# Kernel optimization log

Measured on AMD Instinct MI355X. Metric: run time of the kernel, lower is better.

Reference implementation:

```python
import jax, jax.numpy as jnp
import numpy as np

N, E, D, H, G, L, EF = 50000, 800000, 128, 256, 512, 3, 8
BN_EPS = 1e-5


def _bn(h, g, b):
    # torch BatchNorm1d in training mode: biased batch stats over the node axis
    m = h.mean(0)
    v = h.var(0)
    return g * (h - m) * jax.lax.rsqrt(v + BN_EPS) + b


def setup_inputs() -> dict:
    ks = jax.random.split(jax.random.key(0), 12)
    sc = 0.05
    return {
        "x": jax.random.normal(ks[0], (N, D), jnp.float32),
        "edge_attr": jax.random.normal(ks[1], (E, EF), jnp.float32),
        "vn_emb": jnp.zeros((1, D), jnp.float32),  # init.constant_(0)
        "We": jax.random.normal(ks[2], (L, EF, D)) * sc,
        "be": jnp.zeros((L, D)),
        "W1": jax.random.normal(ks[3], (L, D, H)) * sc,
        "b1": jnp.zeros((L, H)),
        "g1": jnp.ones((L, H)),
        "bt1": jnp.zeros((L, H)),
        "W2": jax.random.normal(ks[4], (L, H, D)) * sc,
        "b2": jnp.zeros((L, D)),
        "gb": jnp.ones((L, D)),
        "bb": jnp.zeros((L, D)),
        "Wv1": jax.random.normal(ks[5], (L - 1, D, H)) * sc,
        "bv1": jnp.zeros((L - 1, H)),
        "gv1": jnp.ones((L - 1, H)),
        "btv1": jnp.zeros((L - 1, H)),
        "Wv2": jax.random.normal(ks[6], (L - 1, H, D)) * sc,
        "bv2": jnp.zeros((L - 1, D)),
        "gv2": jnp.ones((L - 1, D)),
        "btv2": jnp.zeros((L - 1, D)),
        "edge_index": jax.random.randint(ks[7], (2, E), 0, N),
        "batch": jnp.sort(jax.random.randint(ks[8], (N,), 0, G)),
    }


def reference(x, edge_attr, vn_emb, We, be, W1, b1, g1, bt1, W2, b2, gb, bb,
              Wv1, bv1, gv1, btv1, Wv2, bv2, gv2, btv2, edge_index, batch):
    src, dst = edge_index[0], edge_index[1]
    vn = jnp.broadcast_to(vn_emb, (G, D))  # Embedding(1, D) looked up for every graph
    h = x  # node_encoder is None -> encoded_node = x
    for l in range(L):
        h_in = h + vn[batch]                              # virtual-node broadcast (gather)
        e = edge_attr @ We[l] + be[l]                     # per-layer edge encoder
        msg = jax.nn.relu(h_in[src] + e)                  # GIN message, [E, D]
        aggr = jax.ops.segment_sum(msg, dst, num_segments=N)
        z = h_in + aggr                                   # (1+eps)*h + aggr, eps=0
        z = jax.nn.relu(_bn(z @ W1[l] + b1[l], g1[l], bt1[l]))
        h = _bn(z @ W2[l] + b2[l], gb[l], bb[l])          # conv MLP out + outer BatchNorm
        if l < L - 1:
            h = jax.nn.relu(h)                            # dropout ratio 0 -> identity
            pooled = jax.ops.segment_sum(h_in, batch, num_segments=G) + vn
            t = jax.nn.relu(_bn(pooled @ Wv1[l] + bv1[l], gv1[l], btv1[l]))
            vn = jax.nn.relu(_bn(t @ Wv2[l] + bv2[l], gv2[l], btv2[l]))
    return h  # JK == 'last'
```

## Files before the change

### kernel.cpp

```cpp
#include <hip/hip_runtime.h>
#include <hip/hip_bf16.h>

#define N_NODES 50000
#define N_EDGES 800000
#define DIM 128
#define HID 256
#define N_GRAPH 512
#define N_LAYER 3
#define EFEAT 8
#define BN_EPS 1e-5f
#define MAX_GROUPS 240000

typedef unsigned short u16;
typedef unsigned int u32;

using bf16x8_t = short __attribute__((ext_vector_type(8)));
using f32x4_t  = float __attribute__((ext_vector_type(4)));
using f32x2    = float __attribute__((ext_vector_type(2)));
using f32x4v   = float __attribute__((ext_vector_type(4)));


__device__ __forceinline__ void atomic_add_f(float* p, float v) {
    unsafeAtomicAdd(p, v);
}
__device__ __forceinline__ u16 f2bf(float x) {
    union { float f; u32 u; } v; v.f = x;
    u32 r = v.u + 0x7FFF + ((v.u >> 16) & 1);
    return (u16)(r >> 16);
}
__device__ __forceinline__ float bf2f(u16 u) {
    union { u32 i; float f; } v; v.i = (u32)u << 16; return v.f;
}
__device__ __forceinline__ float2 up2(u32 p) {
    return make_float2(bf2f((u16)(p & 0xFFFF)), bf2f((u16)(p >> 16)));
}
__device__ __forceinline__ u32 pk2(float a, float b) {
    return (u32)f2bf(a) | ((u32)f2bf(b) << 16);
}
__device__ __forceinline__ float bflo(u32 u) {
    union { u32 i; float f; } v; v.i = u << 16; return v.f;
}
__device__ __forceinline__ float bfhi(u32 u) {
    union { u32 i; float f; } v; v.i = u & 0xFFFF0000u; return v.f;
}
__device__ __forceinline__ f32x2 up2p(u32 p) {
    union { u32 u[2]; f32x2 f; } v;
    v.u[0] = p << 16;
    v.u[1] = p & 0xFFFF0000u;
    return v.f;
}
__device__ __forceinline__ f32x2 splat2(float x) {
    f32x2 r; r.x = x; r.y = x; return r;
}

__global__ __launch_bounds__(256) void wconv_kernel(
    const float* __restrict__ W1, const float* __restrict__ W2,
    u16* __restrict__ W1t, u16* __restrict__ W2t)
{
    int idx = blockIdx.x * 256 + threadIdx.x;
    if (idx >= 6 * 32768) return;
    int m = idx >> 15;
    int off = idx & 32767;
    int l = m >> 1;
    if ((m & 1) == 0) {
        int r = off >> 8, c = off & 255;
        W1t[(size_t)l * 32768 + c * 128 + r] = f2bf(W1[(size_t)l * 32768 + r * 256 + c]);
    } else {
        int r = off >> 7, c = off & 127;
        W2t[(size_t)l * 32768 + c * 256 + r] = f2bf(W2[(size_t)l * 32768 + r * 128 + c]);
    }
}

__global__ __launch_bounds__(256) void hist_rank_kernel(
    const int* __restrict__ ei, int* __restrict__ deg, int* __restrict__ rank)
{
    int e = blockIdx.x * 256 + threadIdx.x;
    if (e >= N_EDGES) return;
    int dst = ei[N_EDGES + e];
    rank[e] = atomicAdd(&deg[dst], 1);
}

__global__ __launch_bounds__(1024) void scan_kernel(const int* __restrict__ deg, int* __restrict__ grpptr) {
    __shared__ int wsum[16];
    __shared__ int carry;
    int tid = threadIdx.x;
    if (tid == 0) { carry = 0; grpptr[0] = 0; }
    __syncthreads();
    for (int base = 0; base < N_NODES; base += 1024) {
        int i = base + tid;
        int v = (i < N_NODES) ? ((deg[i] + 3) >> 2) : 0;
        int lane = tid & 63, w = tid >> 6;
        int s = v;
        #pragma unroll
        for (int d = 1; d < 64; d <<= 1) { int t = __shfl_up(s, d); if (lane >= d) s += t; }
        if (lane == 63) wsum[w] = s;
        __syncthreads();
        if (tid < 64) {
            int t = (tid < 16) ? wsum[tid] : 0;
            #pragma unroll
            for (int d = 1; d < 16; d <<= 1) { int u = __shfl_up(t, d); if (tid >= d) t += u; }
            if (tid < 16) wsum[tid] = t;
        }
        __syncthreads();
        int excl = (w > 0) ? wsum[w - 1] : 0;
        int incl = s + excl + carry;
        if (i < N_NODES) grpptr[i + 1] = incl;
        __syncthreads();
        if (tid == 0) carry += wsum[15];
        __syncthreads();
    }
}

__global__ __launch_bounds__(256) void scatter_kernel(
    const int* __restrict__ ei, const float* __restrict__ ea,
    const int* __restrict__ rank, const int* __restrict__ grpptr,
    char* __restrict__ rec)
{
    int e = blockIdx.x * 256 + threadIdx.x;
    if (e >= N_EDGES) return;
    int src = __builtin_nontemporal_load(ei + e);
    int dst = __builtin_nontemporal_load(ei + N_EDGES + e);
    int rk  = __builtin_nontemporal_load(rank + e);
    int grp = grpptr[dst] + (rk >> 2);
    int j = rk & 3;
    f32x4v lo = __builtin_nontemporal_load((const f32x4v*)(ea + (size_t)e * EFEAT));
    f32x4v hi = __builtin_nontemporal_load((const f32x4v*)(ea + (size_t)e * EFEAT + 4));
    uint4 q;
    q.x = pk2(lo.x, lo.y); q.y = pk2(lo.z, lo.w);
    q.z = pk2(hi.x, hi.y); q.w = pk2(hi.z, hi.w);
    char* rb = rec + (size_t)grp * 80;
    *(uint4*)(rb + 16 + j * 16) = q;
    *(u32*)(rb + j * 4) = (u32)src << 8;
}

template <bool USEBN, int VNM>
__global__ __launch_bounds__(256) void hin_kernel(
    const float* __restrict__ src,
    const float* __restrict__ sum2, const float* __restrict__ ss2,
    const float* __restrict__ g, const float* __restrict__ b, float invN,
    const int* __restrict__ batch,
    const float* __restrict__ vn_emb,
    const float* __restrict__ vnpre, const float* __restrict__ vsum, const float* __restrict__ vss,
    const float* __restrict__ gv, const float* __restrict__ btv, float invG,
    u16* __restrict__ hin, int total4)
{
    int idx = blockIdx.x * 256 + threadIdx.x;
    if (idx >= total4) return;
    int base = idx * 4;
    int n = base >> 7;
    int c = base & (DIM - 1);
    float4 v = *(const float4*)(src + base);
    float o[4] = {v.x, v.y, v.z, v.w};
    if (USEBN) {
        #pragma unroll
        for (int j = 0; j < 4; ++j) {
            int cj = c + j;
            float m = sum2[cj] * invN;
            float var = ss2[cj] * invN - m * m;
            float r = rsqrtf(var + BN_EPS);
            float a = g[cj] * r;
            o[j] = fmaxf(fmaf(a, o[j], b[cj] - m * a), 0.f);
        }
    }
    int grp = batch[n];
    if (VNM == 0) {
        const float4 w = *(const float4*)(vn_emb + c);
        o[0] += w.x; o[1] += w.y; o[2] += w.z; o[3] += w.w;
    } else {
        const float4 vp = *(const float4*)(vnpre + (size_t)grp * DIM + c);
        float vv[4] = {vp.x, vp.y, vp.z, vp.w};
        #pragma unroll
        for (int j = 0; j < 4; ++j) {
            int cj = c + j;
            float m = vsum[cj] * invG;
            float var = vss[cj] * invG - m * m;
            float r = rsqrtf(var + BN_EPS);
            float a = gv[cj] * r;
            o[j] += fmaxf(fmaf(a, vv[j], btv[cj] - m * a), 0.f);
        }
    }
    uint2 pk;
    pk.x = pk2(o[0], o[1]);
    pk.y = pk2(o[2], o[3]);
    *(uint2*)(hin + base) = pk;
}

__device__ __forceinline__ void edge_term2(
    u32 h, uint4 eq, const f32x2* rW, f32x2 rB, f32x2& acc)
{
    f32x2 ex = rB;
    ex = __builtin_elementwise_fma(splat2(bflo(eq.x)), rW[0], ex);
    ex = __builtin_elementwise_fma(splat2(bfhi(eq.x)), rW[1], ex);
    ex = __builtin_elementwise_fma(splat2(bflo(eq.y)), rW[2], ex);
    ex = __builtin_elementwise_fma(splat2(bfhi(eq.y)), rW[3], ex);
    ex = __builtin_elementwise_fma(splat2(bflo(eq.z)), rW[4], ex);
    ex = __builtin_elementwise_fma(splat2(bfhi(eq.z)), rW[5], ex);
    ex = __builtin_elementwise_fma(splat2(bflo(eq.w)), rW[6], ex);
    ex = __builtin_elementwise_fma(splat2(bfhi(eq.w)), rW[7], ex);
    f32x2 s = up2p(h) + ex;
    s = __builtin_elementwise_max(s, splat2(0.f));
    acc += s;
}

__global__ __launch_bounds__(256) void aggr_kernel(
    const int* __restrict__ grpptr, const int* __restrict__ deg,
    const char* __restrict__ rec,
    const float* __restrict__ Wel, const float* __restrict__ bel,
    const u16* __restrict__ hin, u16* __restrict__ z, int nWaves)
{
    const int lane = threadIdx.x & 63;
    const int cb = lane * 4;
    const int wid0 = (blockIdx.x << 2) + (threadIdx.x >> 6);

    f32x2 rW[EFEAT];
    #pragma unroll
    for (int k = 0; k < EFEAT; ++k) {
        float2 t = *(const float2*)(Wel + k * DIM + lane * 2);
        rW[k].x = t.x; rW[k].y = t.y;
    }
    float2 tb = *(const float2*)(bel + lane * 2);
    f32x2 rB; rB.x = tb.x; rB.y = tb.y;

    const char* hinB = (const char*)hin;

    for (int node = __builtin_amdgcn_readfirstlane(wid0); node < N_NODES; node += nWaves) {
        int g0 = grpptr[node];
        int ng = grpptr[node + 1] - g0;
        int dg = deg[node];
        f32x2 acc = up2p(*(const u32*)(hinB + ((u32)node << 8) + cb));

        if (ng > 0) {
            const char* base = rec + (size_t)g0 * 80;
            uint4 so = *(const uint4*)base;
            uint4 e0 = *(const uint4*)(base + 16);
            uint4 e1 = *(const uint4*)(base + 32);
            uint4 e2 = *(const uint4*)(base + 48);
            uint4 e3 = *(const uint4*)(base + 64);
            u32 h0 = *(const u32*)(hinB + so.x + cb);
            u32 h1 = *(const u32*)(hinB + so.y + cb);
            u32 h2 = *(const u32*)(hinB + so.z + cb);
            u32 h3 = *(const u32*)(hinB + so.w + cb);
            uint4 soA = *(const uint4*)(base + 80);
            const char* pn = base + 80;

            #pragma unroll 1
            for (int c = 0; c < ng - 1; ++c) {
                u32 i0 = *(const u32*)(hinB + soA.x + cb);
                u32 i1 = *(const u32*)(hinB + soA.y + cb);
                u32 i2 = *(const u32*)(hinB + soA.z + cb);
                u32 i3 = *(const u32*)(hinB + soA.w + cb);
                uint4 soN = *(const uint4*)(pn + 80);
                uint4 f0 = *(const uint4*)(pn + 16);
                uint4 f1 = *(const uint4*)(pn + 32);
                uint4 f2 = *(const uint4*)(pn + 48);
                uint4 f3 = *(const uint4*)(pn + 64);
                edge_term2(h0, e0, rW, rB, acc);
                edge_term2(h1, e1, rW, rB, acc);
                edge_term2(h2, e2, rW, rB, acc);
                edge_term2(h3, e3, rW, rB, acc);
                h0 = i0; h1 = i1; h2 = i2; h3 = i3;
                e0 = f0; e1 = f1; e2 = f2; e3 = f3;
                soA = soN;
                pn += 80;
            }
            int valid = dg - (ng - 1) * 4;
            edge_term2(h0, e0, rW, rB, acc);
            if (valid > 1) edge_term2(h1, e1, rW, rB, acc);
            if (valid > 2) edge_term2(h2, e2, rW, rB, acc);
            if (valid > 3) edge_term2(h3, e3, rW, rB, acc);
        }
        *(u32*)(z + ((size_t)node << 7) + lane * 2) = pk2(acc.x, acc.y);
    }
}

template <int MODE, bool CBF16>
__global__ __launch_bounds__(256) void gemm_bf16_kernel(
    const u16* __restrict__ Aa,
    const float* __restrict__ sSum, const float* __restrict__ sSS,
    const float* __restrict__ gA, const float* __restrict__ btA, float invCnt,
    const u16* __restrict__ Bt,
    const float* __restrict__ bias,
    void* __restrict__ CoutV,
    float* __restrict__ outSum, float* __restrict__ outSS,
    int M, int K, int Nc)
{
    constexpr int BM = 128, BN = 128, BK = 128;
    constexpr int LDA = BK + 8;
    __shared__ u16 As[BM * LDA];
    __shared__ u16 Bs[64 * LDA];
    __shared__ float csum[BN], css[BN];

    const int tid = threadIdx.x;
    const int wave = tid >> 6, lane = tid & 63;
    const int row0 = blockIdx.x * BM, col0 = blockIdx.y * BN;
    const int w_m = (wave & 1) * 64, w_n = (wave >> 1) * 32;
    const int quad = lane >> 4, l16 = lane & 15;

    if (tid < BN) { csum[tid] = 0.f; css[tid] = 0.f; }

    f32x4_t acc[4][4];
    #pragma unroll
    for (int mi = 0; mi < 4; ++mi)
        #pragma unroll
        for (int ni = 0; ni < 4; ++ni)
            acc[mi][ni] = (f32x4_t){0.f, 0.f, 0.f, 0.f};

    const int kc = (tid & 15) * 8;
    const int nkt = K / BK;

    for (int kt = 0; kt < nkt; ++kt) {
        float af[8], bf_[8];
        if (MODE == 1) {
            #pragma unroll
            for (int j = 0; j < 8; ++j) {
                int kg = kt * BK + kc + j;
                float m = sSum[kg] * invCnt;
                float var = sSS[kg] * invCnt - m * m;
                float r = rsqrtf(var + BN_EPS);
                float a = gA[kg] * r;
                af[j] = a;
                bf_[j] = btA[kg] - m * a;
            }
        }
        #pragma unroll
        for (int it = 0; it < 8; ++it) {
            int chunk = it * 256 + tid;
            int row = chunk >> 4;
            int gr = row0 + row; if (gr >= M) gr = M - 1;
            uint4 q = *(const uint4*)(Aa + (size_t)gr * K + kt * BK + kc);
            if (MODE == 1) {
                float2 p0 = up2(q.x), p1 = up2(q.y), p2 = up2(q.z), p3 = up2(q.w);
                p0.x = fmaxf(fmaf(af[0], p0.x, bf_[0]), 0.f);
                p0.y = fmaxf(fmaf(af[1], p0.y, bf_[1]), 0.f);
                p1.x = fmaxf(fmaf(af[2], p1.x, bf_[2]), 0.f);
                p1.y = fmaxf(fmaf(af[3], p1.y, bf_[3]), 0.f);
                p2.x = fmaxf(fmaf(af[4], p2.x, bf_[4]), 0.f);
                p2.y = fmaxf(fmaf(af[5], p2.y, bf_[5]), 0.f);
                p3.x = fmaxf(fmaf(af[6], p3.x, bf_[6]), 0.f);
                p3.y = fmaxf(fmaf(af[7], p3.y, bf_[7]), 0.f);
                q.x = pk2(p0.x, p0.y); q.y = pk2(p1.x, p1.y);
                q.z = pk2(p2.x, p2.y); q.w = pk2(p3.x, p3.y);
            }
            *(uint4*)(As + row * LDA + kc) = q;
        }
        #pragma unroll
        for (int half = 0; half < 2; ++half) {
            #pragma unroll
            for (int it = 0; it < 4; ++it) {
                int chunk = it * 256 + tid;
                int n = chunk >> 4;
                uint4 q = *(const uint4*)(Bt + (size_t)(col0 + half * 64 + n) * K + kt * BK + kc);
                *(uint4*)(Bs + n * LDA + kc) = q;
            }
            __syncthreads();
            #pragma unroll
            for (int ks = 0; ks < 4; ++ks) {
                bf16x8_t a_frag[4], b_frag[2];
                #pragma unroll
                for (int mi = 0; mi < 4; ++mi)
                    a_frag[mi] = *(const bf16x8_t*)(As + (w_m + mi * 16 + l16) * LDA + ks * 32 + quad * 8);
                #pragma unroll
                for (int ni = 0; ni < 2; ++ni)
                    b_frag[ni] = *(const bf16x8_t*)(Bs + (w_n + ni * 16 + l16) * LDA + ks * 32 + quad * 8);
                #pragma unroll
                for (int mi = 0; mi < 4; ++mi)
                    #pragma unroll
                    for (int ni = 0; ni < 2; ++ni)
                        acc[mi][half * 2 + ni] = __builtin_amdgcn_mfma_f32_16x16x32_bf16(
                            a_frag[mi], b_frag[ni], acc[mi][half * 2 + ni], 0, 0, 0);
            }
            __syncthreads();
        }
    }

    u16* Cb = (u16*)CoutV;
    float* Cf = (float*)CoutV;
    #pragma unroll
    for (int half = 0; half < 2; ++half)
    #pragma unroll
    for (int ni = 0; ni < 2; ++ni) {
        int ccol = half * 64 + w_n + ni * 16 + l16;
        int col = col0 + ccol;
        float bv = bias[col];
        float s = 0.f, qs = 0.f;
        #pragma unroll
        for (int mi = 0; mi < 4; ++mi) {
            int rbase = row0 + w_m + mi * 16 + quad * 4;
            #pragma unroll
            for (int reg = 0; reg < 4; ++reg) {
                int gr = rbase + reg;
                if (gr < M) {
                    float o = acc[mi][half * 2 + ni][reg] + bv;
                    s += o;
                    qs += o * o;
                    if (CBF16) Cb[(size_t)gr * Nc + col] = f2bf(o);
                    else       Cf[(size_t)gr * Nc + col] = o;
                }
            }
        }
        s += __shfl_xor(s, 16);  s += __shfl_xor(s, 32);
        qs += __shfl_xor(qs, 16);  qs += __shfl_xor(qs, 32);
        if (quad == 0) {
            atomicAdd(&csum[ccol], s);
            atomicAdd(&css[ccol], qs);
        }
    }
    __syncthreads();
    if (tid < BN) {
        atomic_add_f(outSum + col0 + tid, csum[tid]);
        atomic_add_f(outSS + col0 + tid, css[tid]);
    }
}

template <int MODE>
__global__ __launch_bounds__(256) void gemm_kernel(
    const float* __restrict__ Aa,
    const float* __restrict__ sSum, const float* __restrict__ sSS,
    const float* __restrict__ gA, const float* __restrict__ btA, float invCnt,
    const float* __restrict__ B, const float* __restrict__ bias,
    float* __restrict__ Cout, float* __restrict__ outSum, float* __restrict__ outSS,
    int M, int K, int Nc)
{
    __shared__ float As[16][68];
    __shared__ float Bs[16][64];
    __shared__ float alphaS[256], betaS[256];
    __shared__ float csum[64], css[64];

    const int tid = threadIdx.x;
    const int tx = tid & 15, ty = tid >> 4;
    const int row0 = blockIdx.x * 64, col0 = blockIdx.y * 64;

    if (tid < 64) { csum[tid] = 0.f; css[tid] = 0.f; }
    if (MODE == 1) {
        for (int k = tid; k < K; k += 256) {
            float m = sSum[k] * invCnt;
            float var = sSS[k] * invCnt - m * m;
            float r = rsqrtf(var + BN_EPS);
            float a = gA[k] * r;
            alphaS[k] = a;
            betaS[k] = btA[k] - m * a;
        }
    }
    __syncthreads();

    float acc[4][4];
    #pragma unroll
    for (int i = 0; i < 4; ++i)
        #pragma unroll
        for (int j = 0; j < 4; ++j) acc[i][j] = 0.f;

    const int lr = tid >> 2;
    const int lk = (tid & 3) * 4;
    const int bk = tid >> 4;
    const int bc = tx * 4;

    for (int kt = 0; kt < K; kt += 16) {
        int gr = row0 + lr;
        float4 va = make_float4(0.f, 0.f, 0.f, 0.f);
        if (gr < M) {
            va = *(const float4*)(Aa + (size_t)gr * K + kt + lk);
            if (MODE == 1) {
                int k0 = kt + lk;
                va.x = fmaxf(fmaf(alphaS[k0 + 0], va.x, betaS[k0 + 0]), 0.f);
                va.y = fmaxf(fmaf(alphaS[k0 + 1], va.y, betaS[k0 + 1]), 0.f);
                va.z = fmaxf(fmaf(alphaS[k0 + 2], va.z, betaS[k0 + 2]), 0.f);
                va.w = fmaxf(fmaf(alphaS[k0 + 3], va.w, betaS[k0 + 3]), 0.f);
            }
        }
        As[lk + 0][lr] = va.x;
        As[lk + 1][lr] = va.y;
        As[lk + 2][lr] = va.z;
        As[lk + 3][lr] = va.w;
        const float4 vb4 = *(const float4*)(B + (size_t)(kt + bk) * Nc + col0 + bc);
        *(float4*)&Bs[bk][bc] = vb4;
        __syncthreads();
        #pragma unroll
        for (int kk = 0; kk < 16; ++kk) {
            const float4 a4 = *(const float4*)&As[kk][ty * 4];
            const float4 b4 = *(const float4*)&Bs[kk][tx * 4];
            float av[4] = {a4.x, a4.y, a4.z, a4.w};
            float bv4[4] = {b4.x, b4.y, b4.z, b4.w};
            #pragma unroll
            for (int i = 0; i < 4; ++i)
                #pragma unroll
                for (int j = 0; j < 4; ++j)
                    acc[i][j] = fmaf(av[i], bv4[j], acc[i][j]);
        }
        __syncthreads();
    }

    const float4 bvv = *(const float4*)(bias + col0 + tx * 4);
    float bias4[4] = {bvv.x, bvv.y, bvv.z, bvv.w};
    float ps[4] = {0.f, 0.f, 0.f, 0.f};
    float pq[4] = {0.f, 0.f, 0.f, 0.f};
    #pragma unroll
    for (int i = 0; i < 4; ++i) {
        int gr = row0 + ty * 4 + i;
        if (gr < M) {
            float o[4];
            #pragma unroll
            for (int j = 0; j < 4; ++j) {
                o[j] = acc[i][j] + bias4[j];
                ps[j] += o[j];
                pq[j] += o[j] * o[j];
            }
            *(float4*)(Cout + (size_t)gr * Nc + col0 + tx * 4) = make_float4(o[0], o[1], o[2], o[3]);
        }
    }
    #pragma unroll
    for (int j = 0; j < 4; ++j) {
        atomicAdd(&csum[tx * 4 + j], ps[j]);
        atomicAdd(&css[tx * 4 + j], pq[j]);
    }
    __syncthreads();
    if (tid < 64) {
        atomic_add_f(outSum + col0 + tid, csum[tid]);
        atomic_add_f(outSS + col0 + tid, css[tid]);
    }
}

template <int VNM>
__global__ __launch_bounds__(128) void pooled_seg_kernel(
    const u16* __restrict__ hin, const int* __restrict__ batch,
    const float* __restrict__ vn_emb,
    const float* __restrict__ vnpre, const float* __restrict__ vsum, const float* __restrict__ vss,
    const float* __restrict__ gv, const float* __restrict__ btv, float invG,
    float* __restrict__ pooled)
{
    int g = blockIdx.x;
    int c = threadIdx.x;
    int lo = 0, hi = N_NODES;
    while (lo < hi) { int mid = (lo + hi) >> 1; if (batch[mid] < g) lo = mid + 1; else hi = mid; }
    int start = lo;
    hi = N_NODES;
    while (lo < hi) { int mid = (lo + hi) >> 1; if (batch[mid] < g + 1) lo = mid + 1; else hi = mid; }
    int end = lo;
    float acc;
    if (VNM == 0) {
        acc = vn_emb[c];
    } else {
        float m = vsum[c] * invG;
        float var = vss[c] * invG - m * m;
        float r = rsqrtf(var + BN_EPS);
        float a = gv[c] * r;
        acc = fmaxf(fmaf(a, vnpre[(size_t)g * DIM + c], btv[c] - m * a), 0.f);
    }
    float a0 = 0.f, a1 = 0.f, a2 = 0.f, a3 = 0.f;
    int n = start;
    for (; n + 3 < end; n += 4) {
        a0 += bf2f(hin[(size_t)(n + 0) * DIM + c]);
        a1 += bf2f(hin[(size_t)(n + 1) * DIM + c]);
        a2 += bf2f(hin[(size_t)(n + 2) * DIM + c]);
        a3 += bf2f(hin[(size_t)(n + 3) * DIM + c]);
    }
    for (; n < end; ++n) a0 += bf2f(hin[(size_t)n * DIM + c]);
    acc += (a0 + a1) + (a2 + a3);
    pooled[(size_t)g * DIM + c] = acc;
}

__global__ __launch_bounds__(256) void final_bn_kernel(
    float* __restrict__ outp, const float* __restrict__ sum2, const float* __restrict__ ss2,
    const float* __restrict__ g, const float* __restrict__ b, float invN, int total4)
{
    int idx = blockIdx.x * 256 + threadIdx.x;
    if (idx >= total4) return;
    int base = idx * 4;
    int c = base & (DIM - 1);
    float4 v = *(const float4*)(outp + base);
    float o[4] = {v.x, v.y, v.z, v.w};
    #pragma unroll
    for (int j = 0; j < 4; ++j) {
        int cj = c + j;
        float m = sum2[cj] * invN;
        float var = ss2[cj] * invN - m * m;
        float r = rsqrtf(var + BN_EPS);
        float a = g[cj] * r;
        o[j] = fmaf(a, o[j], b[cj] - m * a);
    }
    *(float4*)(outp + base) = make_float4(o[0], o[1], o[2], o[3]);
}

extern "C" void kernel_launch(void* const* d_in, const int* in_sizes, int n_in,
                              void* d_out, int out_size, void* d_ws, size_t ws_size,
                              hipStream_t stream) {
    const float* x         = (const float*)d_in[0];
    const float* edge_attr = (const float*)d_in[1];
    const float* vn_emb    = (const float*)d_in[2];
    const float* We        = (const float*)d_in[3];
    const float* be        = (const float*)d_in[4];
    const float* W1        = (const float*)d_in[5];
    const float* b1        = (const float*)d_in[6];
    const float* g1v       = (const float*)d_in[7];
    const float* bt1       = (const float*)d_in[8];
    const float* W2        = (const float*)d_in[9];
    const float* b2        = (const float*)d_in[10];
    const float* gb        = (const float*)d_in[11];
    const float* bb        = (const float*)d_in[12];
    const float* Wv1       = (const float*)d_in[13];
    const float* bv1       = (const float*)d_in[14];
    const float* gv1       = (const float*)d_in[15];
    const float* btv1      = (const float*)d_in[16];
    const float* Wv2       = (const float*)d_in[17];
    const float* bv2       = (const float*)d_in[18];
    const float* gv2       = (const float*)d_in[19];
    const float* btv2      = (const float*)d_in[20];
    const int* edge_index  = (const int*)d_in[21];
    const int* batch       = (const int*)d_in[22];
    float* outp = (float*)d_out;

    auto au = [](size_t x) { return (x + 255) & ~(size_t)255; };
    char* p = (char*)d_ws;
    u16* h_in   = (u16*)p;  p += au((size_t)N_NODES * DIM * 2);
    u16* z_bf   = (u16*)p;  p += au((size_t)N_NODES * DIM * 2);
    u16* c1_bf  = (u16*)p;  p += au((size_t)N_NODES * HID * 2);
    u16* W1t    = (u16*)p;  p += au((size_t)3 * 32768 * 2);
    u16* W2t    = (u16*)p;  p += au((size_t)3 * 32768 * 2);
    float* pooled = (float*)p;  p += au((size_t)N_GRAPH * DIM * 4);
    float* tpre   = (float*)p;  p += au((size_t)N_GRAPH * HID * 4);
    float* vnpre  = (float*)p;  p += au((size_t)N_GRAPH * DIM * 4);
    float* stats  = (float*)p;  p += au(2048 * 4);
    float* sum1 = stats,        *ss1 = stats + 256;
    float* sum2 = stats + 512,  *ss2 = stats + 640;
    float* vsum1 = stats + 768, *vss1 = stats + 1024;
    float* vsum2 = stats + 1280, *vss2 = stats + 1408;
    int* grpptr = (int*)p;  p += au((size_t)(N_NODES + 1) * 4);
    int* deg    = (int*)p;  p += au((size_t)N_NODES * 4);
    int* rank   = (int*)p;  p += au((size_t)N_EDGES * 4);
    char* rec   = p;

    const size_t REC_BYTES = (size_t)MAX_GROUPS * 80 + 256;
    const float invN = 1.0f / (float)N_NODES;
    const float invG = 1.0f / (float)N_GRAPH;
    const int total4 = N_NODES * DIM / 4;

    hipMemsetAsync(deg, 0, N_NODES * sizeof(int), stream);
    hipMemsetAsync(rec, 0, REC_BYTES, stream);
    hist_rank_kernel<<<(N_EDGES + 255) / 256, 256, 0, stream>>>(edge_index, deg, rank);
    scan_kernel<<<1, 1024, 0, stream>>>(deg, grpptr);
    scatter_kernel<<<(N_EDGES + 255) / 256, 256, 0, stream>>>(
        edge_index, edge_attr, rank, grpptr, rec);
    wconv_kernel<<<768, 256, 0, stream>>>(W1, W2, W1t, W2t);

    const int AGGR_BLOCKS = 2048;
    const int nWaves = AGGR_BLOCKS * 4;

    for (int l = 0; l < N_LAYER; ++l) {
        if (l == 0)
            hin_kernel<false, 0><<<(total4 + 255) / 256, 256, 0, stream>>>(
                x, nullptr, nullptr, nullptr, nullptr, 0.f, batch,
                vn_emb, nullptr, nullptr, nullptr, nullptr, nullptr, 0.f,
                h_in, total4);
        else
            hin_kernel<true, 1><<<(total4 + 255) / 256, 256, 0, stream>>>(
                outp, sum2, ss2, gb + (size_t)(l - 1) * DIM, bb + (size_t)(l - 1) * DIM, invN, batch,
                nullptr, vnpre, vsum2, vss2,
                gv2 + (size_t)(l - 1) * DIM, btv2 + (size_t)(l - 1) * DIM, invG,
                h_in, total4);

        if (l == 0)
            pooled_seg_kernel<0><<<N_GRAPH, 128, 0, stream>>>(
                h_in, batch, vn_emb, nullptr, nullptr, nullptr, nullptr, nullptr, 0.f, pooled);
        else if (l < N_LAYER - 1)
            pooled_seg_kernel<1><<<N_GRAPH, 128, 0, stream>>>(
                h_in, batch, nullptr, vnpre, vsum2, vss2,
                gv2 + (size_t)(l - 1) * DIM, btv2 + (size_t)(l - 1) * DIM, invG, pooled);

        hipMemsetAsync(stats, 0, 2048 * sizeof(float), stream);

        aggr_kernel<<<AGGR_BLOCKS, 256, 0, stream>>>(
            grpptr, deg, rec, We + (size_t)l * EFEAT * DIM, be + (size_t)l * DIM,
            h_in, z_bf, nWaves);

        dim3 g1d((N_NODES + 127) / 128, HID / 128);
        gemm_bf16_kernel<0, true><<<g1d, 256, 0, stream>>>(
            z_bf, nullptr, nullptr, nullptr, nullptr, 0.f,
            W1t + (size_t)l * 32768, b1 + (size_t)l * HID,
            (void*)c1_bf, sum1, ss1, N_NODES, DIM, HID);

        dim3 g2d((N_NODES + 127) / 128, DIM / 128);
        gemm_bf16_kernel<1, false><<<g2d, 256, 0, stream>>>(
            c1_bf, sum1, ss1, g1v + (size_t)l * HID, bt1 + (size_t)l * HID, invN,
            W2t + (size_t)l * 32768, b2 + (size_t)l * DIM,
            (void*)outp, sum2, ss2, N_NODES, HID, DIM);

        if (l < N_LAYER - 1) {
            dim3 g3d(N_GRAPH / 64, HID / 64);
            gemm_kernel<0><<<g3d, 256, 0, stream>>>(
                pooled, nullptr, nullptr, nullptr, nullptr, 0.f,
                Wv1 + (size_t)l * DIM * HID, bv1 + (size_t)l * HID,
                tpre, vsum1, vss1, N_GRAPH, DIM, HID);

            dim3 g4d(N_GRAPH / 64, DIM / 64);
            gemm_kernel<1><<<g4d, 256, 0, stream>>>(
                tpre, vsum1, vss1, gv1 + (size_t)l * HID, btv1 + (size_t)l * HID, invG,
                Wv2 + (size_t)l * HID * DIM, bv2 + (size_t)l * DIM,
                vnpre, vsum2, vss2, N_GRAPH, HID, DIM);
        }
    }

    final_bn_kernel<<<(total4 + 255) / 256, 256, 0, stream>>>(
        outp, sum2, ss2, gb + (size_t)2 * DIM, bb + (size_t)2 * DIM, invN, total4);
}
```

Before: 779.1 us.

## Balance edge aggregation by group count per wave, using padded fp32 edge records

Work in the aggregation kernel is now split by edge groups instead of by node stride. A new kernel binary-searches the group prefix array so that each wave gets an equal share of groups, and the wave walks consecutive nodes in one software-pipelined stream. Edge features are kept as fp32 in 144-byte records. Padding slots point to an extra h_in row filled with large negative bf16 values, so the ReLU zeroes them and the per-node valid-count branches go away. The deg and rank scratch arrays now reuse the z and c1 buffers, and the rec memset becomes a pad-init kernel. The cost is more bytes per edge record and a few extra setup launches.

```diff
diff --git a/kernel.cpp b/kernel.cpp
--- a/kernel.cpp
+++ b/kernel.cpp
@@ -10,6 +10,7 @@
 #define EFEAT 8
 #define BN_EPS 1e-5f
 #define MAX_GROUPS 240000
+#define AGGR_WAVES 8192
 
 typedef unsigned short u16;
 typedef unsigned int u32;
@@ -36,12 +37,6 @@
 }
 __device__ __forceinline__ u32 pk2(float a, float b) {
     return (u32)f2bf(a) | ((u32)f2bf(b) << 16);
-}
-__device__ __forceinline__ float bflo(u32 u) {
-    union { u32 i; float f; } v; v.i = u << 16; return v.f;
-}
-__device__ __forceinline__ float bfhi(u32 u) {
-    union { u32 i; float f; } v; v.i = u & 0xFFFF0000u; return v.f;
 }
 __device__ __forceinline__ f32x2 up2p(u32 p) {
     union { u32 u[2]; f32x2 f; } v;
@@ -111,6 +106,26 @@
     }
 }
 
+__global__ __launch_bounds__(256) void padinit_kernel(uint4* __restrict__ rec4, int nslots) {
+    int i = blockIdx.x * 256 + threadIdx.x;
+    if (i >= nslots) return;
+    int g = i / 9;
+    int j = i - g * 9;
+    uint4 v;
+    if (j == 0) {
+        u32 s = (u32)N_NODES << 8;
+        v = make_uint4(s, s, s, s);
+    } else {
+        v = make_uint4(0u, 0u, 0u, 0u);
+    }
+    rec4[i] = v;
+}
+
+__global__ void negrow_kernel(u16* __restrict__ hin) {
+    int l = threadIdx.x;
+    *(u32*)(hin + (size_t)N_NODES * DIM + l * 2) = 0xFF7FFF7Fu;
+}
+
 __global__ __launch_bounds__(256) void scatter_kernel(
     const int* __restrict__ ei, const float* __restrict__ ea,
     const int* __restrict__ rank, const int* __restrict__ grpptr,
@@ -125,12 +140,23 @@
     int j = rk & 3;
     f32x4v lo = __builtin_nontemporal_load((const f32x4v*)(ea + (size_t)e * EFEAT));
     f32x4v hi = __builtin_nontemporal_load((const f32x4v*)(ea + (size_t)e * EFEAT + 4));
-    uint4 q;
-    q.x = pk2(lo.x, lo.y); q.y = pk2(lo.z, lo.w);
-    q.z = pk2(hi.x, hi.y); q.w = pk2(hi.z, hi.w);
-    char* rb = rec + (size_t)grp * 80;
-    *(uint4*)(rb + 16 + j * 16) = q;
+    char* rb = rec + (size_t)grp * 144;
     *(u32*)(rb + j * 4) = (u32)src << 8;
+    *(f32x4v*)(rb + 16 + j * 32) = lo;
+    *(f32x4v*)(rb + 32 + j * 32) = hi;
+}
+
+__global__ __launch_bounds__(256) void wstart_kernel(
+    const int* __restrict__ grpptr, int* __restrict__ wstart)
+{
+    int w = blockIdx.x * 256 + threadIdx.x;
+    if (w > AGGR_WAVES) return;
+    if (w == AGGR_WAVES) { wstart[w] = N_NODES; return; }
+    int Gt = grpptr[N_NODES];
+    int q = (int)(((long long)w * Gt) / AGGR_WAVES);
+    int lo = 0, hi = N_NODES;
+    while (lo < hi) { int mid = (lo + hi) >> 1; if (grpptr[mid] < q) lo = mid + 1; else hi = mid; }
+    wstart[w] = lo;
 }
 
 template <bool USEBN, int VNM>
@@ -185,32 +211,32 @@
     *(uint2*)(hin + base) = pk;
 }
 
-__device__ __forceinline__ void edge_term2(
-    u32 h, uint4 eq, const f32x2* rW, f32x2 rB, f32x2& acc)
+__device__ __forceinline__ void edge_term_f(
+    u32 h, f32x4v ea, f32x4v eb, const f32x2* rW, f32x2 rB, f32x2& acc)
 {
     f32x2 ex = rB;
-    ex = __builtin_elementwise_fma(splat2(bflo(eq.x)), rW[0], ex);
-    ex = __builtin_elementwise_fma(splat2(bfhi(eq.x)), rW[1], ex);
-    ex = __builtin_elementwise_fma(splat2(bflo(eq.y)), rW[2], ex);
-    ex = __builtin_elementwise_fma(splat2(bfhi(eq.y)), rW[3], ex);
-    ex = __builtin_elementwise_fma(splat2(bflo(eq.z)), rW[4], ex);
-    ex = __builtin_elementwise_fma(splat2(bfhi(eq.z)), rW[5], ex);
-    ex = __builtin_elementwise_fma(splat2(bflo(eq.w)), rW[6], ex);
-    ex = __builtin_elementwise_fma(splat2(bfhi(eq.w)), rW[7], ex);
+    ex = __builtin_elementwise_fma(splat2(ea.x), rW[0], ex);
+    ex = __builtin_elementwise_fma(splat2(ea.y), rW[1], ex);
+    ex = __builtin_elementwise_fma(splat2(ea.z), rW[2], ex);
+    ex = __builtin_elementwise_fma(splat2(ea.w), rW[3], ex);
+    ex = __builtin_elementwise_fma(splat2(eb.x), rW[4], ex);
+    ex = __builtin_elementwise_fma(splat2(eb.y), rW[5], ex);
+    ex = __builtin_elementwise_fma(splat2(eb.z), rW[6], ex);
+    ex = __builtin_elementwise_fma(splat2(eb.w), rW[7], ex);
     f32x2 s = up2p(h) + ex;
     s = __builtin_elementwise_max(s, splat2(0.f));
     acc += s;
 }
 
 __global__ __launch_bounds__(256) void aggr_kernel(
-    const int* __restrict__ grpptr, const int* __restrict__ deg,
-    const char* __restrict__ rec,
+    const int* __restrict__ grpptr, const char* __restrict__ rec,
     const float* __restrict__ Wel, const float* __restrict__ bel,
-    const u16* __restrict__ hin, u16* __restrict__ z, int nWaves)
+    const u16* __restrict__ hin, u16* __restrict__ z,
+    const int* __restrict__ wstart)
 {
     const int lane = threadIdx.x & 63;
     const int cb = lane * 4;
-    const int wid0 = (blockIdx.x << 2) + (threadIdx.x >> 6);
+    const int wid = __builtin_amdgcn_readfirstlane((blockIdx.x << 2) + (threadIdx.x >> 6));
 
     f32x2 rW[EFEAT];
     #pragma unroll
@@ -222,54 +248,78 @@
     f32x2 rB; rB.x = tb.x; rB.y = tb.y;
 
     const char* hinB = (const char*)hin;
-
-    for (int node = __builtin_amdgcn_readfirstlane(wid0); node < N_NODES; node += nWaves) {
-        int g0 = grpptr[node];
-        int ng = grpptr[node + 1] - g0;
-        int dg = deg[node];
-        f32x2 acc = up2p(*(const u32*)(hinB + ((u32)node << 8) + cb));
-
-        if (ng > 0) {
-            const char* base = rec + (size_t)g0 * 80;
-            uint4 so = *(const uint4*)base;
-            uint4 e0 = *(const uint4*)(base + 16);
-            uint4 e1 = *(const uint4*)(base + 32);
-            uint4 e2 = *(const uint4*)(base + 48);
-            uint4 e3 = *(const uint4*)(base + 64);
-            u32 h0 = *(const u32*)(hinB + so.x + cb);
-            u32 h1 = *(const u32*)(hinB + so.y + cb);
-            u32 h2 = *(const u32*)(hinB + so.z + cb);
-            u32 h3 = *(const u32*)(hinB + so.w + cb);
-            uint4 soA = *(const uint4*)(base + 80);
-            const char* pn = base + 80;
-
-            #pragma unroll 1
-            for (int c = 0; c < ng - 1; ++c) {
-                u32 i0 = *(const u32*)(hinB + soA.x + cb);
-                u32 i1 = *(const u32*)(hinB + soA.y + cb);
-                u32 i2 = *(const u32*)(hinB + soA.z + cb);
-                u32 i3 = *(const u32*)(hinB + soA.w + cb);
-                uint4 soN = *(const uint4*)(pn + 80);
-                uint4 f0 = *(const uint4*)(pn + 16);
-                uint4 f1 = *(const uint4*)(pn + 32);
-                uint4 f2 = *(const uint4*)(pn + 48);
-                uint4 f3 = *(const uint4*)(pn + 64);
-                edge_term2(h0, e0, rW, rB, acc);
-                edge_term2(h1, e1, rW, rB, acc);
-                edge_term2(h2, e2, rW, rB, acc);
-                edge_term2(h3, e3, rW, rB, acc);
-                h0 = i0; h1 = i1; h2 = i2; h3 = i3;
-                e0 = f0; e1 = f1; e2 = f2; e3 = f3;
-                soA = soN;
-                pn += 80;
+    int n = wstart[wid];
+    const int n1 = wstart[wid + 1];
+
+    while (n < n1 && grpptr[n + 1] == grpptr[n]) {
+        f32x2 a0 = up2p(*(const u32*)(hinB + ((u32)n << 8) + cb));
+        *(u32*)(z + ((size_t)n << 7) + lane * 2) = pk2(a0.x, a0.y);
+        ++n;
+    }
+    if (n < n1) {
+        int g = grpptr[n];
+        const int gTot = grpptr[n1];
+        int gEnd = grpptr[n + 1];
+        f32x2 acc = up2p(*(const u32*)(hinB + ((u32)n << 8) + cb));
+        const char* rb = rec + (size_t)g * 144;
+
+        uint4 so = *(const uint4*)rb;
+        u32 h0 = *(const u32*)(hinB + so.x + cb);
+        u32 h1 = *(const u32*)(hinB + so.y + cb);
+        u32 h2 = *(const u32*)(hinB + so.z + cb);
+        u32 h3 = *(const u32*)(hinB + so.w + cb);
+        f32x4v e0a = *(const f32x4v*)(rb + 16);
+        f32x4v e0b = *(const f32x4v*)(rb + 32);
+        f32x4v e1a = *(const f32x4v*)(rb + 48);
+        f32x4v e1b = *(const f32x4v*)(rb + 64);
+        f32x4v e2a = *(const f32x4v*)(rb + 80);
+        f32x4v e2b = *(const f32x4v*)(rb + 96);
+        f32x4v e3a = *(const f32x4v*)(rb + 112);
+        f32x4v e3b = *(const f32x4v*)(rb + 128);
+        uint4 soN = *(const uint4*)(rb + 144);
+
+        #pragma unroll 2
+        for (; g < gTot; ++g, rb += 144) {
+            u32 i0 = *(const u32*)(hinB + soN.x + cb);
+            u32 i1 = *(const u32*)(hinB + soN.y + cb);
+            u32 i2 = *(const u32*)(hinB + soN.z + cb);
+            u32 i3 = *(const u32*)(hinB + soN.w + cb);
+            f32x4v f0a = *(const f32x4v*)(rb + 160);
+            f32x4v f0b = *(const f32x4v*)(rb + 176);
+            f32x4v f1a = *(const f32x4v*)(rb + 192);
+            f32x4v f1b = *(const f32x4v*)(rb + 208);
+            f32x4v f2a = *(const f32x4v*)(rb + 224);
+            f32x4v f2b = *(const f32x4v*)(rb + 240);
+            f32x4v f3a = *(const f32x4v*)(rb + 256);
+            f32x4v f3b = *(const f32x4v*)(rb + 272);
+            uint4 soNN = *(const uint4*)(rb + 288);
+            edge_term_f(h0, e0a, e0b, rW, rB, acc);
+            edge_term_f(h1, e1a, e1b, rW, rB, acc);
+            edge_term_f(h2, e2a, e2b, rW, rB, acc);
+            edge_term_f(h3, e3a, e3b, rW, rB, acc);
+            h0 = i0; h1 = i1; h2 = i2; h3 = i3;
+            e0a = f0a; e0b = f0b; e1a = f1a; e1b = f1b;
+            e2a = f2a; e2b = f2b; e3a = f3a; e3b = f3b;
+            soN = soNN;
+            if (g + 1 == gEnd) {
+                *(u32*)(z + ((size_t)n << 7) + lane * 2) = pk2(acc.x, acc.y);
+                ++n;
+                if (g + 1 < gTot) {
+                    while (grpptr[n + 1] == grpptr[n]) {
+                        f32x2 a0 = up2p(*(const u32*)(hinB + ((u32)n << 8) + cb));
+                        *(u32*)(z + ((size_t)n << 7) + lane * 2) = pk2(a0.x, a0.y);
+                        ++n;
+                    }
+                    acc = up2p(*(const u32*)(hinB + ((u32)n << 8) + cb));
+                    gEnd = grpptr[n + 1];
+                }
             }
-            int valid = dg - (ng - 1) * 4;
-            edge_term2(h0, e0, rW, rB, acc);
-            if (valid > 1) edge_term2(h1, e1, rW, rB, acc);
-            if (valid > 2) edge_term2(h2, e2, rW, rB, acc);
-            if (valid > 3) edge_term2(h3, e3, rW, rB, acc);
-        }
-        *(u32*)(z + ((size_t)node << 7) + lane * 2) = pk2(acc.x, acc.y);
+        }
+    }
+    while (n < n1) {
+        f32x2 a0 = up2p(*(const u32*)(hinB + ((u32)n << 8) + cb));
+        *(u32*)(z + ((size_t)n << 7) + lane * 2) = pk2(a0.x, a0.y);
+        ++n;
     }
 }
 
@@ -610,7 +660,7 @@
 
     auto au = [](size_t x) { return (x + 255) & ~(size_t)255; };
     char* p = (char*)d_ws;
-    u16* h_in   = (u16*)p;  p += au((size_t)N_NODES * DIM * 2);
+    u16* h_in   = (u16*)p;  p += au((size_t)(N_NODES + 1) * DIM * 2);
     u16* z_bf   = (u16*)p;  p += au((size_t)N_NODES * DIM * 2);
     u16* c1_bf  = (u16*)p;  p += au((size_t)N_NODES * HID * 2);
     u16* W1t    = (u16*)p;  p += au((size_t)3 * 32768 * 2);
@@ -624,25 +674,29 @@
     float* vsum1 = stats + 768, *vss1 = stats + 1024;
     float* vsum2 = stats + 1280, *vss2 = stats + 1408;
     int* grpptr = (int*)p;  p += au((size_t)(N_NODES + 1) * 4);
-    int* deg    = (int*)p;  p += au((size_t)N_NODES * 4);
-    int* rank   = (int*)p;  p += au((size_t)N_EDGES * 4);
-    char* rec   = p;
-
-    const size_t REC_BYTES = (size_t)MAX_GROUPS * 80 + 256;
+    int* wstart = (int*)p;  p += au((size_t)(AGGR_WAVES + 1) * 4);
+    char* rec   = p;        p += au((size_t)(MAX_GROUPS + 4) * 144);
+    int* deg  = (int*)z_bf;
+    int* rank = (int*)c1_bf;
+
     const float invN = 1.0f / (float)N_NODES;
     const float invG = 1.0f / (float)N_GRAPH;
     const int total4 = N_NODES * DIM / 4;
 
     hipMemsetAsync(deg, 0, N_NODES * sizeof(int), stream);
-    hipMemsetAsync(rec, 0, REC_BYTES, stream);
     hist_rank_kernel<<<(N_EDGES + 255) / 256, 256, 0, stream>>>(edge_index, deg, rank);
     scan_kernel<<<1, 1024, 0, stream>>>(deg, grpptr);
+    {
+        int nslots = (MAX_GROUPS + 4) * 9;
+        padinit_kernel<<<(nslots + 255) / 256, 256, 0, stream>>>((uint4*)rec, nslots);
+    }
+    negrow_kernel<<<1, 64, 0, stream>>>(h_in);
     scatter_kernel<<<(N_EDGES + 255) / 256, 256, 0, stream>>>(
         edge_index, edge_attr, rank, grpptr, rec);
+    wstart_kernel<<<(AGGR_WAVES + 256) / 256, 256, 0, stream>>>(grpptr, wstart);
     wconv_kernel<<<768, 256, 0, stream>>>(W1, W2, W1t, W2t);
 
-    const int AGGR_BLOCKS = 2048;
-    const int nWaves = AGGR_BLOCKS * 4;
+    const int AGGR_BLOCKS = AGGR_WAVES / 4;
 
     for (int l = 0; l < N_LAYER; ++l) {
         if (l == 0)
@@ -668,8 +722,8 @@
         hipMemsetAsync(stats, 0, 2048 * sizeof(float), stream);
 
         aggr_kernel<<<AGGR_BLOCKS, 256, 0, stream>>>(
-            grpptr, deg, rec, We + (size_t)l * EFEAT * DIM, be + (size_t)l * DIM,
-            h_in, z_bf, nWaves);
+            grpptr, rec, We + (size_t)l * EFEAT * DIM, be + (size_t)l * DIM,
+            h_in, z_bf, wstart);
 
         dim3 g1d((N_NODES + 127) / 128, HID / 128);
         gemm_bf16_kernel<0, true><<<g1d, 256, 0, stream>>>(
```

New measurement: 786.1 us. Within noise of the previous version (+0.9%).
